# Kernel optimization log

Hardware: AMD Instinct MI355X
Metric: run time of the kernel (lower is better)

## Reference

```python
import jax, jax.numpy as jnp
import numpy as np

KNN = 16          # graph_knn
TWIN = 2          # graph_temporal_window
B, S, M, C, D = 16, 2048, 128, 32, 512
V1 = 1024         # vocab_l1


def setup_inputs() -> dict:
    key = jax.random.key(0)
    ks = jax.random.split(key, 9)
    return {
        'coords': jax.random.normal(ks[0], (B, S, 2), jnp.float32),
        'tokens_l1': jax.random.randint(ks[1], (B, S), 0, V1, dtype=jnp.int32),
        'step_mask': jax.random.randint(ks[2], (B, S), 0, 2, dtype=jnp.int32),
        'step_to_mid': jax.random.randint(ks[3], (B, S), 0, M, dtype=jnp.int32),
        'mid_mask': jax.random.randint(ks[4], (B, M), 0, 2, dtype=jnp.int32),
        'step_to_coarse': jax.random.randint(ks[5], (B, S), 0, C, dtype=jnp.int32),
        'coarse_mask': jax.random.randint(ks[6], (B, C), 0, 2, dtype=jnp.int32),
        'mid_hidden': jax.random.normal(ks[7], (B, M, D), jnp.float32),
        'W_flow': jax.random.normal(ks[8], (D, D), jnp.float32) * 0.02,
    }


def _step_graph(coords, valid, tok):
    # coords [S,2], valid [S] bool, tok [S] int -> [S,S] bool adjacency
    s = valid.shape[0]
    rank = jnp.cumsum(valid.astype(jnp.int32)) - 1  # rank among valid positions
    pv = valid[:, None] & valid[None, :]
    diag = jnp.eye(s, dtype=bool) & valid[:, None]
    # temporal window is over *valid-position order* (index t in valid_idx)
    temporal = pv & (jnp.abs(rank[:, None] - rank[None, :]) <= TWIN)
    same = pv & (tok[:, None] == tok[None, :])
    # knn over valid points (squared euclidean; same ordering as cdist p=2)
    sq = jnp.sum(coords * coords, axis=-1)
    d2 = sq[:, None] + sq[None, :] - 2.0 * (coords @ coords.T)
    d2 = jnp.where(pv, jnp.maximum(d2, 0.0), jnp.inf)
    k = KNN + 1  # self included, as in torch.topk(largest=False) with k=knn+1
    negv, idx = jax.lax.top_k(-d2, k)            # [S,k]
    finite = jnp.isfinite(negv)                  # drop padded inf cols (vlen < k)
    knn_e = jnp.zeros((s, s), bool).at[jnp.arange(s)[:, None], idx].max(finite)
    knn_e = knn_e | knn_e.T
    return diag | temporal | same | knn_e


def _attn_mask(valid, s2m, mmask, s2c, cmask):
    # valid [S], s2m [S] int, mmask [M], s2c [S] int, cmask [C] -> [T,T] bool
    s, m, c = valid.shape[0], mmask.shape[0], cmask.shape[0]
    step_block = valid[:, None] & valid[None, :]  # step_attention_window == 0
    m_ok = valid & (s2m >= 0) & (s2m < m) & mmask[jnp.clip(s2m, 0, m - 1)]
    e_sm = (jnp.arange(m)[None, :] == s2m[:, None]) & m_ok[:, None]  # [S,M]
    c_ok = valid & (s2c >= 0) & (s2c < c) & cmask[jnp.clip(s2c, 0, c - 1)]
    e_sc = (jnp.arange(c)[None, :] == s2c[:, None]) & c_ok[:, None]  # [S,C]
    top = jnp.concatenate([step_block, e_sm, e_sc], axis=1)
    mid = jnp.concatenate([e_sm.T, jnp.diag(mmask), jnp.zeros((m, c), bool)], axis=1)
    coa = jnp.concatenate([e_sc.T, jnp.zeros((c, m), bool), jnp.diag(cmask)], axis=1)
    a = jnp.concatenate([top, mid, coa], axis=0)
    return a | jnp.eye(s + m + c, dtype=bool)  # full diagonal set True


def reference(coords, tokens_l1, step_mask, step_to_mid, mid_mask,
              step_to_coarse, coarse_mask, mid_hidden, W_flow):
    valid = step_mask > 0
    mmask = mid_mask > 0
    cmask = coarse_mask > 0
    graph = jax.vmap(_step_graph)(coords, valid, tokens_l1)
    attn = jax.vmap(_attn_mask)(valid, step_to_mid, mmask, step_to_coarse, cmask)
    # meso_flow_logits: proj = flow_proj(mid_hidden) (Linear, no bias)
    proj = jnp.einsum('bmd,ed->bme', mid_hidden, W_flow)
    logits = jnp.einsum('bmd,bnd->bmn', proj, proj) / np.float32(np.sqrt(D))
    pair = mmask[:, :, None] & mmask[:, None, :]
    logits = jnp.where(pair, logits, 0.0)
    return graph, attn, logits
```

## Files before the change

kernel.cpp:

```cpp
#include <hip/hip_runtime.h>
#include <stdint.h>

typedef unsigned int u32;
typedef unsigned long long u64;

#define BB 16
#define SS 2048
#define MM 128
#define CC 32
#define DD 512
#define TT (SS + MM + CC)
#define KSEL 17

__global__ __launch_bounds__(256) void prep_kernel(
    const int* __restrict__ step_mask, const int* __restrict__ tokens,
    const int* __restrict__ s2m, const int* __restrict__ mid_mask,
    const int* __restrict__ s2c, const int* __restrict__ coarse_mask,
    u32* __restrict__ colkey, int* __restrict__ midtgt, int* __restrict__ coatgt)
{
    const int b = blockIdx.x, t = threadIdx.x;
    __shared__ int sums[256];
    const int base = b * SS + t * 8;
    int v[8]; int loc = 0;
#pragma unroll
    for (int e = 0; e < 8; ++e) { v[e] = step_mask[base + e] > 0; loc += v[e]; }
    sums[t] = loc;
    __syncthreads();
    int x = loc;
    for (int off = 1; off < 256; off <<= 1) {
        int y = (t >= off) ? sums[t - off] : 0;
        __syncthreads();
        x += y; sums[t] = x;
        __syncthreads();
    }
    int run = x - loc;
#pragma unroll
    for (int e = 0; e < 8; ++e) {
        const int idx = base + e;
        run += v[e];
        u32 key = 0u;
        if (v[e]) {
            int rank = run - 1;
            key = 0x80000000u | ((u32)tokens[idx] << 11) | (u32)(rank & 0x7FF);
        }
        colkey[idx] = key;
        int sm = s2m[idx];
        midtgt[idx] = (v[e] && sm >= 0 && sm < MM && mid_mask[b * MM + sm] > 0) ? sm : -1;
        int sc = s2c[idx];
        coatgt[idx] = (v[e] && sc >= 0 && sc < CC && coarse_mask[b * CC + sc] > 0) ? sc : -1;
    }
}

__global__ __launch_bounds__(256) void knn_kernel(
    const float* __restrict__ coords, const u32* __restrict__ colkey,
    u32* __restrict__ knnbits)
{
    const int wave = (blockIdx.x << 2) | (threadIdx.x >> 6);
    const int lane = threadIdx.x & 63;
    const int b = wave >> 11;
    const int i = wave & 2047;
    const u32 key_i = colkey[b * SS + i];
    if (!(key_i & 0x80000000u)) return;

    const float2* cb = (const float2*)coords + (size_t)b * SS;
    const float2 ci = cb[i];
    const float sqi = __fadd_rn(__fmul_rn(ci.x, ci.x), __fmul_rn(ci.y, ci.y));

    u64 packed[32];
#pragma unroll
    for (int s = 0; s < 32; ++s) {
        const int j = (s << 6) | lane;
        const float2 cj = cb[j];
        const u32 kj = colkey[b * SS + j];
        const float sqj = __fadd_rn(__fmul_rn(cj.x, cj.x), __fmul_rn(cj.y, cj.y));
        const float dot = __builtin_fmaf(ci.y, cj.y, __fmul_rn(ci.x, cj.x));
        float d2 = __fsub_rn(__fadd_rn(sqi, sqj), __fmul_rn(2.0f, dot));
        d2 = fmaxf(d2, 0.0f);
        const u64 p = ((u64)__float_as_uint(d2) << 32) | (u32)(j + 1);
        packed[s] = (kj & 0x80000000u) ? p : ~0ull;
    }

    u64 prev = 0ull;
    u32* rowi = knnbits + ((size_t)(b * SS + i) << 6);
    for (int r = 0; r < KSEL; ++r) {
        u64 best = ~0ull;
#pragma unroll
        for (int s = 0; s < 32; ++s) {
            const u64 p = packed[s];
            const bool c = (p > prev) && (p < best);
            best = c ? p : best;
        }
#pragma unroll
        for (int m = 1; m < 64; m <<= 1) {
            const u64 o = __shfl_xor(best, m, 64);
            best = (o < best) ? o : best;
        }
        if (best == ~0ull) break;
        prev = best;
        if (lane == 0) {
            const u32 j = (u32)best - 1u;
            atomicOr(&rowi[j >> 5], 1u << (j & 31));
            atomicOr(&knnbits[((size_t)(b * SS + j) << 6) + (i >> 5)], 1u << (i & 31));
        }
    }
}

__device__ __forceinline__ float graph_elem(u32 key_i, int ri, u32 kj, u32 knnw,
                                            int i, int j)
{
    if (!(kj & 0x80000000u)) return 0.0f;
    int rj = (int)(kj & 0x7FFu);
    int dr = ri - rj; dr = dr < 0 ? -dr : dr;
    const bool same = ((key_i ^ kj) & 0x1FF800u) == 0u;
    const bool knn = (knnw >> (j & 31)) & 1u;
    return (dr <= 2 || same || knn || (i == j)) ? 1.0f : 0.0f;
}

__global__ __launch_bounds__(256) void graph_kernel(
    const u32* __restrict__ colkey, const u32* __restrict__ knnbits,
    float* __restrict__ out)
{
    const int tid = blockIdx.x * 256 + threadIdx.x;
    const int j4 = tid & 511;
    const int i = (tid >> 9) & 2047;
    const int b = tid >> 20;
    const int jb = j4 << 2;
    const u32 key_i = colkey[(b << 11) | i];
    float4 o;
    if (!(key_i & 0x80000000u)) {
        o = make_float4(0.f, 0.f, 0.f, 0.f);
    } else {
        const uint4 kj = *(const uint4*)(colkey + (b << 11) + jb);
        const u32 knnw = knnbits[(((size_t)((b << 11) | i)) << 6) + (jb >> 5)];
        const int ri = (int)(key_i & 0x7FFu);
        o.x = graph_elem(key_i, ri, kj.x, knnw, i, jb);
        o.y = graph_elem(key_i, ri, kj.y, knnw, i, jb + 1);
        o.z = graph_elem(key_i, ri, kj.z, knnw, i, jb + 2);
        o.w = graph_elem(key_i, ri, kj.w, knnw, i, jb + 3);
    }
    *(float4*)(out + ((size_t)tid << 2)) = o;
}

__global__ __launch_bounds__(256) void attn_kernel(
    const u32* __restrict__ colkey, const int* __restrict__ midtgt,
    const int* __restrict__ coatgt, float* __restrict__ out)
{
    const int tid = blockIdx.x * 256 + threadIdx.x;
    const int c4 = tid % 552;
    const int rt = tid / 552;
    const int r = rt % TT;
    const int b = rt / TT;
    const int cb = c4 << 2;
    float4 o;
    if (r < SS) {
        if (cb < SS) {
            const u32 vr = colkey[b * SS + r] >> 31;
            const uint4 kc = *(const uint4*)(colkey + b * SS + cb);
            o.x = ((vr & (kc.x >> 31)) | (u32)(r == cb))     ? 1.f : 0.f;
            o.y = ((vr & (kc.y >> 31)) | (u32)(r == cb + 1)) ? 1.f : 0.f;
            o.z = ((vr & (kc.z >> 31)) | (u32)(r == cb + 2)) ? 1.f : 0.f;
            o.w = ((vr & (kc.w >> 31)) | (u32)(r == cb + 3)) ? 1.f : 0.f;
        } else if (cb < SS + MM) {
            const int mt = midtgt[b * SS + r];
            const int m0 = cb - SS;
            o.x = (mt == m0)     ? 1.f : 0.f;
            o.y = (mt == m0 + 1) ? 1.f : 0.f;
            o.z = (mt == m0 + 2) ? 1.f : 0.f;
            o.w = (mt == m0 + 3) ? 1.f : 0.f;
        } else {
            const int ct = coatgt[b * SS + r];
            const int c0 = cb - SS - MM;
            o.x = (ct == c0)     ? 1.f : 0.f;
            o.y = (ct == c0 + 1) ? 1.f : 0.f;
            o.z = (ct == c0 + 2) ? 1.f : 0.f;
            o.w = (ct == c0 + 3) ? 1.f : 0.f;
        }
    } else if (r < SS + MM) {
        const int m = r - SS;
        if (cb < SS) {
            const int4 mt = *(const int4*)(midtgt + b * SS + cb);
            o.x = (mt.x == m) ? 1.f : 0.f;
            o.y = (mt.y == m) ? 1.f : 0.f;
            o.z = (mt.z == m) ? 1.f : 0.f;
            o.w = (mt.w == m) ? 1.f : 0.f;
        } else {
            o.x = (cb == r)     ? 1.f : 0.f;
            o.y = (cb + 1 == r) ? 1.f : 0.f;
            o.z = (cb + 2 == r) ? 1.f : 0.f;
            o.w = (cb + 3 == r) ? 1.f : 0.f;
        }
    } else {
        const int cc = r - SS - MM;
        if (cb < SS) {
            const int4 ct = *(const int4*)(coatgt + b * SS + cb);
            o.x = (ct.x == cc) ? 1.f : 0.f;
            o.y = (ct.y == cc) ? 1.f : 0.f;
            o.z = (ct.z == cc) ? 1.f : 0.f;
            o.w = (ct.w == cc) ? 1.f : 0.f;
        } else {
            o.x = (cb == r)     ? 1.f : 0.f;
            o.y = (cb + 1 == r) ? 1.f : 0.f;
            o.z = (cb + 2 == r) ? 1.f : 0.f;
            o.w = (cb + 3 == r) ? 1.f : 0.f;
        }
    }
    *(float4*)(out + (size_t)rt * TT + cb) = o;
}

__device__ __forceinline__ float dot4(float acc, const float4& va, const float4& vb)
{
    return fmaf(va.x, vb.x, fmaf(va.y, vb.y, fmaf(va.z, vb.z, fmaf(va.w, vb.w, acc))));
}

__global__ __launch_bounds__(256) void proj_kernel(
    const float* __restrict__ mid_hidden, const float* __restrict__ W,
    float* __restrict__ proj)
{
    const int b = blockIdx.z;
    const int m0 = blockIdx.y * 32 + (threadIdx.x >> 4) * 2;
    const int e0 = blockIdx.x * 64 + (threadIdx.x & 15) * 4;
    const float* a0 = mid_hidden + (size_t)(b * MM + m0) * DD;
    const float* a1 = a0 + DD;
    const float* w0 = W + (size_t)e0 * DD;
    const float* w1 = w0 + DD;
    const float* w2 = w1 + DD;
    const float* w3 = w2 + DD;
    float acc[2][4] = {};
    for (int k = 0; k < DD; k += 4) {
        const float4 va0 = *(const float4*)(a0 + k);
        const float4 va1 = *(const float4*)(a1 + k);
        const float4 vw0 = *(const float4*)(w0 + k);
        const float4 vw1 = *(const float4*)(w1 + k);
        const float4 vw2 = *(const float4*)(w2 + k);
        const float4 vw3 = *(const float4*)(w3 + k);
        acc[0][0] = dot4(acc[0][0], va0, vw0); acc[0][1] = dot4(acc[0][1], va0, vw1);
        acc[0][2] = dot4(acc[0][2], va0, vw2); acc[0][3] = dot4(acc[0][3], va0, vw3);
        acc[1][0] = dot4(acc[1][0], va1, vw0); acc[1][1] = dot4(acc[1][1], va1, vw1);
        acc[1][2] = dot4(acc[1][2], va1, vw2); acc[1][3] = dot4(acc[1][3], va1, vw3);
    }
    float* p0 = proj + (size_t)(b * MM + m0) * DD + e0;
    float* p1 = p0 + DD;
    p0[0] = acc[0][0]; p0[1] = acc[0][1]; p0[2] = acc[0][2]; p0[3] = acc[0][3];
    p1[0] = acc[1][0]; p1[1] = acc[1][1]; p1[2] = acc[1][2]; p1[3] = acc[1][3];
}

__global__ __launch_bounds__(256) void logits_kernel(
    const float* __restrict__ proj, const int* __restrict__ mid_mask,
    float* __restrict__ out)
{
    const int b = blockIdx.z;
    const int m0 = blockIdx.y * 32 + (threadIdx.x >> 4) * 2;
    const int n0 = blockIdx.x * 32 + (threadIdx.x & 15) * 2;
    const float* pm0 = proj + (size_t)(b * MM + m0) * DD;
    const float* pm1 = pm0 + DD;
    const float* pn0 = proj + (size_t)(b * MM + n0) * DD;
    const float* pn1 = pn0 + DD;
    float acc[2][2] = {};
    for (int k = 0; k < DD; k += 4) {
        const float4 a0 = *(const float4*)(pm0 + k);
        const float4 a1 = *(const float4*)(pm1 + k);
        const float4 q0 = *(const float4*)(pn0 + k);
        const float4 q1 = *(const float4*)(pn1 + k);
        acc[0][0] = dot4(acc[0][0], a0, q0); acc[0][1] = dot4(acc[0][1], a0, q1);
        acc[1][0] = dot4(acc[1][0], a1, q0); acc[1][1] = dot4(acc[1][1], a1, q1);
    }
    const bool qm0 = mid_mask[b * MM + m0] > 0;
    const bool qm1 = mid_mask[b * MM + m0 + 1] > 0;
    const bool qn0 = mid_mask[b * MM + n0] > 0;
    const bool qn1 = mid_mask[b * MM + n0 + 1] > 0;
    const float sc = 22.62741699796952f;
    float* o = out + (size_t)(b * MM + m0) * MM + n0;
    o[0]       = (qm0 && qn0) ? acc[0][0] / sc : 0.f;
    o[1]       = (qm0 && qn1) ? acc[0][1] / sc : 0.f;
    o[MM]      = (qm1 && qn0) ? acc[1][0] / sc : 0.f;
    o[MM + 1]  = (qm1 && qn1) ? acc[1][1] / sc : 0.f;
}

extern "C" void kernel_launch(void* const* d_in, const int* in_sizes, int n_in,
                              void* d_out, int out_size, void* d_ws, size_t ws_size,
                              hipStream_t stream)
{
    const float* coords      = (const float*)d_in[0];
    const int*   tokens      = (const int*)d_in[1];
    const int*   step_mask   = (const int*)d_in[2];
    const int*   s2m         = (const int*)d_in[3];
    const int*   mid_mask    = (const int*)d_in[4];
    const int*   s2c         = (const int*)d_in[5];
    const int*   coarse_mask = (const int*)d_in[6];
    const float* mid_hidden  = (const float*)d_in[7];
    const float* W_flow      = (const float*)d_in[8];

    float* graph_out  = (float*)d_out;
    float* attn_out   = graph_out + (size_t)BB * SS * SS;
    float* logits_out = attn_out + (size_t)BB * TT * TT;

    char* ws = (char*)d_ws;
    u32* colkey  = (u32*)ws;
    int* midtgt  = (int*)(ws + (128 << 10));
    int* coatgt  = (int*)(ws + (256 << 10));
    u32* knnbits = (u32*)(ws + (384 << 10));
    const size_t knn_bytes  = (size_t)BB * SS * 64 * 4;
    const size_t proj_off   = (384 << 10) + knn_bytes;
    const size_t proj_bytes = (size_t)BB * MM * DD * 4;
    float* proj = (ws_size >= proj_off + proj_bytes) ? (float*)(ws + proj_off)
                                                     : (float*)knnbits;

    hipMemsetAsync(knnbits, 0, knn_bytes, stream);
    prep_kernel<<<BB, 256, 0, stream>>>(step_mask, tokens, s2m, mid_mask,
                                        s2c, coarse_mask, colkey, midtgt, coatgt);
    knn_kernel<<<(BB * SS) / 4, 256, 0, stream>>>(coords, colkey, knnbits);
    graph_kernel<<<(BB * SS * (SS / 4)) / 256, 256, 0, stream>>>(colkey, knnbits, graph_out);
    attn_kernel<<<(BB * TT * (TT / 4)) / 256, 256, 0, stream>>>(colkey, midtgt, coatgt, attn_out);
    proj_kernel<<<dim3(DD / 64, MM / 32, BB), 256, 0, stream>>>(mid_hidden, W_flow, proj);
    logits_kernel<<<dim3(MM / 32, MM / 32, BB), 256, 0, stream>>>(proj, mid_mask, logits_out);
}
```

Measured before the change: 417.7 us.

## Compact valid points for KNN, use nontemporal output stores and kernel zeroing

The prep kernel now writes a compacted list of valid positions and coordinates plus the valid count, so the KNN kernel only scans valid candidates and skips whole 64-wide slots beyond the count. Selection packs distance, rank and position into one 64-bit key and removes each winner from the register list, replacing the strictly-greater-than-previous filter. Graph and attention outputs use nontemporal stores to avoid cache pollution on large write streams. The memset is replaced by a custom zero kernel. This needs extra workspace and a different key packing, and ties are ordered by rank instead of index, which gives the same order because rank follows index order.

```diff
diff --git a/kernel.cpp b/kernel.cpp
--- a/kernel.cpp
+++ b/kernel.cpp
@@ -12,11 +12,36 @@
 #define TT (SS + MM + CC)
 #define KSEL 17
 
+#define OFF_COLKEY 0
+#define OFF_MIDTGT (128 << 10)
+#define OFF_COATGT (256 << 10)
+#define OFF_VPOS   (384 << 10)
+#define OFF_VLEN   (512 << 10)
+#define OFF_VCOORD (520 << 10)
+#define OFF_KNN    (776 << 10)
+#define KNN_BYTES  ((size_t)BB * SS * 64 * 4)
+#define OFF_PROJ   ((size_t)(776 << 10) + KNN_BYTES)
+#define PROJ_BYTES ((size_t)BB * MM * DD * 4)
+
+typedef float nfloat4 __attribute__((ext_vector_type(4)));
+__device__ __forceinline__ void st_nt_f4(float* p, float4 v) {
+    nfloat4 nv; nv.x = v.x; nv.y = v.y; nv.z = v.z; nv.w = v.w;
+    __builtin_nontemporal_store(nv, (nfloat4*)p);
+}
+
+__global__ __launch_bounds__(256) void zero_kernel(uint4* __restrict__ p)
+{
+    const int tid = blockIdx.x * 256 + threadIdx.x;
+    p[tid] = make_uint4(0u, 0u, 0u, 0u);
+}
+
 __global__ __launch_bounds__(256) void prep_kernel(
+    const float* __restrict__ coords,
     const int* __restrict__ step_mask, const int* __restrict__ tokens,
     const int* __restrict__ s2m, const int* __restrict__ mid_mask,
     const int* __restrict__ s2c, const int* __restrict__ coarse_mask,
-    u32* __restrict__ colkey, int* __restrict__ midtgt, int* __restrict__ coatgt)
+    u32* __restrict__ colkey, int* __restrict__ midtgt, int* __restrict__ coatgt,
+    u32* __restrict__ vpos, int* __restrict__ vlen, float2* __restrict__ vcoord)
 {
     const int b = blockIdx.x, t = threadIdx.x;
     __shared__ int sums[256];
@@ -33,15 +58,20 @@
         x += y; sums[t] = x;
         __syncthreads();
     }
+    if (t == 255) vlen[b] = x;
     int run = x - loc;
+    const float2* cb = (const float2*)coords + (size_t)b * SS;
 #pragma unroll
     for (int e = 0; e < 8; ++e) {
         const int idx = base + e;
+        const int pos = t * 8 + e;
         run += v[e];
         u32 key = 0u;
         if (v[e]) {
             int rank = run - 1;
             key = 0x80000000u | ((u32)tokens[idx] << 11) | (u32)(rank & 0x7FF);
+            vpos[b * SS + rank] = (u32)pos;
+            vcoord[b * SS + rank] = cb[pos];
         }
         colkey[idx] = key;
         int sm = s2m[idx];
@@ -53,7 +83,8 @@
 
 __global__ __launch_bounds__(256) void knn_kernel(
     const float* __restrict__ coords, const u32* __restrict__ colkey,
-    u32* __restrict__ knnbits)
+    const u32* __restrict__ vpos, const int* __restrict__ vlen,
+    const float2* __restrict__ vcoord, u32* __restrict__ knnbits)
 {
     const int wave = (blockIdx.x << 2) | (threadIdx.x >> 6);
     const int lane = threadIdx.x & 63;
@@ -62,6 +93,7 @@
     const u32 key_i = colkey[b * SS + i];
     if (!(key_i & 0x80000000u)) return;
 
+    const int n = vlen[b];
     const float2* cb = (const float2*)coords + (size_t)b * SS;
     const float2 ci = cb[i];
     const float sqi = __fadd_rn(__fmul_rn(ci.x, ci.x), __fmul_rn(ci.y, ci.y));
@@ -69,26 +101,27 @@
     u64 packed[32];
 #pragma unroll
     for (int s = 0; s < 32; ++s) {
-        const int j = (s << 6) | lane;
-        const float2 cj = cb[j];
-        const u32 kj = colkey[b * SS + j];
-        const float sqj = __fadd_rn(__fmul_rn(cj.x, cj.x), __fmul_rn(cj.y, cj.y));
-        const float dot = __builtin_fmaf(ci.y, cj.y, __fmul_rn(ci.x, cj.x));
-        float d2 = __fsub_rn(__fadd_rn(sqi, sqj), __fmul_rn(2.0f, dot));
-        d2 = fmaxf(d2, 0.0f);
-        const u64 p = ((u64)__float_as_uint(d2) << 32) | (u32)(j + 1);
-        packed[s] = (kj & 0x80000000u) ? p : ~0ull;
-    }
-
-    u64 prev = 0ull;
-    u32* rowi = knnbits + ((size_t)(b * SS + i) << 6);
-    for (int r = 0; r < KSEL; ++r) {
+        packed[s] = ~0ull;
+        if ((s << 6) < n) {
+            const int r = (s << 6) | lane;
+            if (r < n) {
+                const float2 cj = vcoord[(b << 11) + r];
+                const u32 pos = vpos[(b << 11) + r];
+                const float sqj = __fadd_rn(__fmul_rn(cj.x, cj.x), __fmul_rn(cj.y, cj.y));
+                const float dot = __builtin_fmaf(ci.y, cj.y, __fmul_rn(ci.x, cj.x));
+                float d2 = __fsub_rn(__fadd_rn(sqi, sqj), __fmul_rn(2.0f, dot));
+                d2 = fmaxf(d2, 0.0f);
+                packed[s] = ((u64)__float_as_uint(d2) << 22) | ((u32)r << 11) | pos;
+            }
+        }
+    }
+
+    u32* rowi = knnbits + ((size_t)((b << 11) | i) << 6);
+    for (int rnd = 0; rnd < KSEL; ++rnd) {
         u64 best = ~0ull;
 #pragma unroll
         for (int s = 0; s < 32; ++s) {
-            const u64 p = packed[s];
-            const bool c = (p > prev) && (p < best);
-            best = c ? p : best;
+            if ((s << 6) < n) best = (packed[s] < best) ? packed[s] : best;
         }
 #pragma unroll
         for (int m = 1; m < 64; m <<= 1) {
@@ -96,11 +129,19 @@
             best = (o < best) ? o : best;
         }
         if (best == ~0ull) break;
-        prev = best;
+        const u32 lo = (u32)best;
+        const u32 wrank = (lo >> 11) & 0x7FFu;
+        const u32 wposn = lo & 0x7FFu;
+#pragma unroll
+        for (int s = 0; s < 32; ++s) {
+            if ((s << 6) < n) {
+                if (wrank == (u32)((s << 6) | lane)) packed[s] = ~0ull;
+            }
+        }
         if (lane == 0) {
-            const u32 j = (u32)best - 1u;
-            atomicOr(&rowi[j >> 5], 1u << (j & 31));
-            atomicOr(&knnbits[((size_t)(b * SS + j) << 6) + (i >> 5)], 1u << (i & 31));
+            atomicOr(&rowi[wposn >> 5], 1u << (wposn & 31));
+            atomicOr(&knnbits[((size_t)((b << 11) | wposn) << 6) + (i >> 5)],
+                     1u << (i & 31));
         }
     }
 }
@@ -138,7 +179,7 @@
         o.z = graph_elem(key_i, ri, kj.z, knnw, i, jb + 2);
         o.w = graph_elem(key_i, ri, kj.w, knnw, i, jb + 3);
     }
-    *(float4*)(out + ((size_t)tid << 2)) = o;
+    st_nt_f4(out + ((size_t)tid << 2), o);
 }
 
 __global__ __launch_bounds__(256) void attn_kernel(
@@ -204,7 +245,7 @@
             o.w = (cb + 3 == r) ? 1.f : 0.f;
         }
     }
-    *(float4*)(out + (size_t)rt * TT + cb) = o;
+    st_nt_f4(out + (size_t)rt * TT + cb, o);
 }
 
 __device__ __forceinline__ float dot4(float acc, const float4& va, const float4& vb)
@@ -295,20 +336,22 @@
     float* logits_out = attn_out + (size_t)BB * TT * TT;
 
     char* ws = (char*)d_ws;
-    u32* colkey  = (u32*)ws;
-    int* midtgt  = (int*)(ws + (128 << 10));
-    int* coatgt  = (int*)(ws + (256 << 10));
-    u32* knnbits = (u32*)(ws + (384 << 10));
-    const size_t knn_bytes  = (size_t)BB * SS * 64 * 4;
-    const size_t proj_off   = (384 << 10) + knn_bytes;
-    const size_t proj_bytes = (size_t)BB * MM * DD * 4;
-    float* proj = (ws_size >= proj_off + proj_bytes) ? (float*)(ws + proj_off)
+    u32*    colkey  = (u32*)(ws + OFF_COLKEY);
+    int*    midtgt  = (int*)(ws + OFF_MIDTGT);
+    int*    coatgt  = (int*)(ws + OFF_COATGT);
+    u32*    vpos    = (u32*)(ws + OFF_VPOS);
+    int*    vlen    = (int*)(ws + OFF_VLEN);
+    float2* vcoord  = (float2*)(ws + OFF_VCOORD);
+    u32*    knnbits = (u32*)(ws + OFF_KNN);
+    float* proj = (ws_size >= OFF_PROJ + PROJ_BYTES) ? (float*)(ws + OFF_PROJ)
                                                      : (float*)knnbits;
 
-    hipMemsetAsync(knnbits, 0, knn_bytes, stream);
-    prep_kernel<<<BB, 256, 0, stream>>>(step_mask, tokens, s2m, mid_mask,
-                                        s2c, coarse_mask, colkey, midtgt, coatgt);
-    knn_kernel<<<(BB * SS) / 4, 256, 0, stream>>>(coords, colkey, knnbits);
+    zero_kernel<<<(int)(KNN_BYTES / (256 * 16)), 256, 0, stream>>>((uint4*)knnbits);
+    prep_kernel<<<BB, 256, 0, stream>>>(coords, step_mask, tokens, s2m, mid_mask,
+                                        s2c, coarse_mask, colkey, midtgt, coatgt,
+                                        vpos, vlen, vcoord);
+    knn_kernel<<<(BB * SS) / 4, 256, 0, stream>>>(coords, colkey, vpos, vlen,
+                                                  vcoord, knnbits);
     graph_kernel<<<(BB * SS * (SS / 4)) / 256, 256, 0, stream>>>(colkey, knnbits, graph_out);
     attn_kernel<<<(BB * TT * (TT / 4)) / 256, 256, 0, stream>>>(colkey, midtgt, coatgt, attn_out);
     proj_kernel<<<dim3(DD / 64, MM / 32, BB), 256, 0, stream>>>(mid_hidden, W_flow, proj);
```

New measurement: 456.9 us. 1.09x slower.
